# Kernel optimization log

Measured on AMD Instinct MI355X. Metric: run time of the kernel, lower is better.

The kernel has to match this reference:

```python
import jax, jax.numpy as jnp
import numpy as np

D_MODEL = 1024
N_HEADS = 16


def setup_inputs() -> dict:
    key = jax.random.key(0)
    ks = jax.random.split(key, 5)
    sigma = (1.0 / D_MODEL) ** 0.5
    return {
        "x": jax.random.normal(ks[0], (4, 2048, D_MODEL), dtype=jnp.float32),
        "W_q": jax.random.normal(ks[1], (D_MODEL, D_MODEL), dtype=jnp.float32) * sigma,
        "W_k": jax.random.normal(ks[2], (D_MODEL, D_MODEL), dtype=jnp.float32) * sigma,
        "W_v": jax.random.normal(ks[3], (D_MODEL, D_MODEL), dtype=jnp.float32) * sigma,
        "W_o": jax.random.normal(ks[4], (D_MODEL, D_MODEL), dtype=jnp.float32) * sigma,
    }


def reference(x, W_q, W_k, W_v, W_o):
    b, s, d = x.shape
    h = N_HEADS
    d_h = d // h
    # Projections: original does einsum('d_out dim, ... dim -> ... d_out') == x @ W.T
    def proj(W):
        y = jnp.einsum('bsd,ed->bse', x, W)
        # ... seq (head d_h) -> ... head seq d_h
        return y.reshape(b, s, h, d_h).transpose(0, 2, 1, 3)
    Q, K, V = proj(W_q), proj(W_k), proj(W_v)
    scale = 1.0 / jnp.sqrt(jnp.asarray(d_h, dtype=x.dtype))
    scores = jnp.einsum('bhqd,bhkd->bhqk', Q, K) * scale  # [b,h,s,s]
    causal = jnp.tril(jnp.ones((s, s), dtype=bool))
    scores = jnp.where(causal, scores, -jnp.inf)
    attn = jax.nn.softmax(scores, axis=-1)
    out = jnp.einsum('bhqk,bhkd->bhqd', attn, V)  # [b,h,s,d_h]
    out = out.transpose(0, 2, 1, 3).reshape(b, s, d)
    # einsum(Temp, W_o, '... dim1, dim dim1 -> ... dim') == Temp @ W_o.T
    return jnp.einsum('bse,de->bsd', out, W_o)
```

## Files before the change

### kernel.cpp

```cpp
#include <hip/hip_runtime.h>

typedef __attribute__((ext_vector_type(8))) short s16x8;
typedef __attribute__((ext_vector_type(4))) short s16x4;
typedef __attribute__((ext_vector_type(4))) float f32x4;
typedef unsigned short u16;
typedef unsigned int u32;
typedef unsigned long long u64;

__device__ __forceinline__ u16 f2bf(float f) {
  unsigned u = __builtin_bit_cast(unsigned, f);
  return (u16)((u + 0x7fffu + ((u >> 16) & 1u)) >> 16);
}

#define QSCALE 0.18033688011112042f

__device__ __forceinline__ void gld16(const u16* g, u16* l) {
  __builtin_amdgcn_global_load_lds(
      (const __attribute__((address_space(1))) void*)g,
      (__attribute__((address_space(3))) void*)l, 16, 0, 0);
}

__device__ __forceinline__ u32 pack_trunc(float a, float b) {
  return __builtin_amdgcn_perm(__builtin_bit_cast(u32, b),
                               __builtin_bit_cast(u32, a), 0x07060302u);
}

__global__ __launch_bounds__(256)
void cvt_bf16(const float* __restrict__ src, u16* __restrict__ dst, int n8)
{
  const int i = blockIdx.x * 256 + threadIdx.x;
  if (i < n8) {
    f32x4 a = ((const f32x4*)src)[2 * i];
    f32x4 b = ((const f32x4*)src)[2 * i + 1];
    s16x8 pk;
    pk[0] = (short)f2bf(a[0]); pk[1] = (short)f2bf(a[1]);
    pk[2] = (short)f2bf(a[2]); pk[3] = (short)f2bf(a[3]);
    pk[4] = (short)f2bf(b[0]); pk[5] = (short)f2bf(b[1]);
    pk[6] = (short)f2bf(b[2]); pk[7] = (short)f2bf(b[3]);
    ((s16x8*)dst)[i] = pk;
  }
}

template<bool OUT_QKV>
__global__ __launch_bounds__(256)
void gemm97(const u16* __restrict__ A,
            const u16* __restrict__ B0, const u16* __restrict__ B1,
            const u16* __restrict__ B2,
            u16* __restrict__ o0, u16* __restrict__ o1, u16* __restrict__ o2,
            float* __restrict__ oF)
{
  const int by = blockIdx.x;
  const int bx = blockIdx.y;
  const int bz = blockIdx.z;
  const u16* B = (bz == 0) ? B0 : ((bz == 1) ? B1 : B2);
  u16* oQ = (bz == 0) ? o0 : ((bz == 1) ? o1 : o2);

  __shared__ u16 As[128 * 32];
  __shared__ u16 Bs[128 * 32];

  const int tid  = threadIdx.x;
  const int w    = tid >> 6;
  const int lane = tid & 63;
  const int quad = lane >> 4;
  const int l15  = lane & 15;
  const int wm   = (w >> 1) * 64;
  const int wn   = (w & 1) * 64;

  const int arb  = w * 32;
  const int srow = lane >> 2;
  const int scol = (lane & 3) * 8;
  const u16* ga = A + (size_t)(by * 128 + arb + srow) * 1024 + scol;
  const u16* gb = B + (size_t)(bx * 128 + arb + srow) * 1024 + scol;
  u16* la0 = &As[arb * 32];
  u16* la1 = &As[(arb + 16) * 32];
  u16* lb0 = &Bs[arb * 32];
  u16* lb1 = &Bs[(arb + 16) * 32];

  f32x4 acc[4][4];
  #pragma unroll
  for (int i = 0; i < 4; ++i)
    #pragma unroll
    for (int j = 0; j < 4; ++j)
      acc[i][j] = (f32x4){0.f, 0.f, 0.f, 0.f};

  for (int k0 = 0; k0 < 1024; k0 += 32) {
    gld16(ga + k0,               la0);
    gld16(ga + k0 + 16 * 1024,   la1);
    gld16(gb + k0,               lb0);
    gld16(gb + k0 + 16 * 1024,   lb1);
    __syncthreads();

    s16x8 af[4], bf[4];
    #pragma unroll
    for (int i = 0; i < 4; ++i)
      af[i] = *(const s16x8*)&As[(wm + i * 16 + l15) * 32 + quad * 8];
    #pragma unroll
    for (int i = 0; i < 4; ++i)
      bf[i] = *(const s16x8*)&Bs[(wn + i * 16 + l15) * 32 + quad * 8];
    #pragma unroll
    for (int mt = 0; mt < 4; ++mt)
      #pragma unroll
      for (int nt = 0; nt < 4; ++nt)
        acc[mt][nt] = __builtin_amdgcn_mfma_f32_16x16x32_bf16(
            af[mt], bf[nt], acc[mt][nt], 0, 0, 0);
    __syncthreads();
  }

  #pragma unroll
  for (int mt = 0; mt < 4; ++mt)
    #pragma unroll
    for (int nt = 0; nt < 4; ++nt)
      #pragma unroll
      for (int r = 0; r < 4; ++r) {
        const int row = by * 128 + wm + mt * 16 + quad * 4 + r;
        const int col = bx * 128 + wn + nt * 16 + l15;
        float v = acc[mt][nt][r];
        if (OUT_QKV) {
          if (bz == 0) v *= QSCALE;
          const int b = row >> 11, s = row & 2047, hh = col >> 6, d = col & 63;
          oQ[(size_t)(b * 16 + hh) * 131072 + s * 64 + d] = f2bf(v);
        } else {
          oF[(size_t)row * 1024 + col] = v;
        }
      }
}

__global__ __launch_bounds__(256)
void vtrans(const u16* __restrict__ Vb, u16* __restrict__ VT)
{
  const int st = blockIdx.x;
  const int bh = blockIdx.y;
  __shared__ u16 T[64 * 72];
  const int tid = threadIdx.x;
  const size_t base = (size_t)bh * 131072;
  #pragma unroll
  for (int p = 0; p < 2; ++p) {
    const int idx = tid + p * 256;
    const int row = idx >> 3;
    const int col = (idx & 7) * 8;
    s16x8 v = *(const s16x8*)(Vb + base + (size_t)(st * 64 + row) * 64 + col);
    #pragma unroll
    for (int e = 0; e < 8; ++e) T[(col + e) * 72 + row] = v[e];
  }
  __syncthreads();
  #pragma unroll
  for (int p = 0; p < 2; ++p) {
    const int idx = tid + p * 256;
    const int drow = idx >> 3;
    const int scol = (idx & 7) * 8;
    *(s16x8*)(VT + base + (size_t)drow * 2048 + st * 64 + scol) =
        *(const s16x8*)&T[drow * 72 + scol];
  }
}

#define ATTN_STEP(t, Pw, qtt)                                                  \
  do {                                                                         \
    f32x4 S[4];                                                                \
    _Pragma("unroll")                                                          \
    for (int nt = 0; nt < 4; ++nt) {                                           \
      s16x8 b0 = *(const s16x8*)&Ks[(nt * 16 + l15) * 72 + quad * 8];          \
      s16x8 b1 = *(const s16x8*)&Ks[(nt * 16 + l15) * 72 + 32 + quad * 8];     \
      f32x4 z = (f32x4){0.f, 0.f, 0.f, 0.f};                                   \
      z = __builtin_amdgcn_mfma_f32_16x16x32_bf16(aq[t][0], b0, z, 0, 0, 0);   \
      z = __builtin_amdgcn_mfma_f32_16x16x32_bf16(aq[t][1], b1, z, 0, 0, 0);   \
      S[nt] = z;                                                               \
    }                                                                          \
    if (j == (qtt)) {                                                          \
      _Pragma("unroll")                                                        \
      for (int nt = 0; nt < 4; ++nt)                                           \
        _Pragma("unroll")                                                      \
        for (int r = 0; r < 4; ++r) {                                          \
          const int kg = 4 * l15 + nt;                                         \
          const int qg = w * 16 + quad * 4 + r;                                \
          if (kg > qg) S[nt][r] = -1e30f;                                      \
        }                                                                      \
    }                                                                          \
    _Pragma("unroll")                                                          \
    for (int r = 0; r < 4; ++r) {                                              \
      float rm = fmaxf(fmaxf(S[0][r], S[1][r]), fmaxf(S[2][r], S[3][r]));      \
      _Pragma("unroll")                                                        \
      for (int off = 1; off < 16; off <<= 1)                                   \
        rm = fmaxf(rm, __shfl_xor(rm, off, 64));                               \
      const float mold = mi[t][r];                                             \
      const float mnew = fmaxf(mold, rm);                                      \
      const float alpha = __builtin_amdgcn_exp2f(mold - mnew);                 \
      mi[t][r] = mnew;                                                         \
      const float p0 = __builtin_amdgcn_exp2f(S[0][r] - mnew);                 \
      const float p1 = __builtin_amdgcn_exp2f(S[1][r] - mnew);                 \
      const float p2 = __builtin_amdgcn_exp2f(S[2][r] - mnew);                 \
      const float p3 = __builtin_amdgcn_exp2f(S[3][r] - mnew);                 \
      liacc[t][r] *= alpha;                                                    \
      _Pragma("unroll")                                                        \
      for (int dt = 0; dt < 4; ++dt) O[t][dt][r] *= alpha;                     \
      const u64 pk = (u64)pack_trunc(p0, p1) |                                 \
                     ((u64)pack_trunc(p2, p3) << 32);                          \
      *(u64*)&(Pw)[(quad * 4 + r) * 72 + 4 * l15] = pk;                        \
    }                                                                          \
    s16x8 a0 = *(const s16x8*)&(Pw)[l15 * 72 + quad * 8];                      \
    s16x8 a1 = *(const s16x8*)&(Pw)[l15 * 72 + 32 + quad * 8];                 \
    liacc[t] = __builtin_amdgcn_mfma_f32_16x16x32_bf16(a0, ones, liacc[t], 0, 0, 0); \
    liacc[t] = __builtin_amdgcn_mfma_f32_16x16x32_bf16(a1, ones, liacc[t], 0, 0, 0); \
    _Pragma("unroll")                                                          \
    for (int dt = 0; dt < 4; ++dt) {                                           \
      s16x8 b0 = *(const s16x8*)&Vt[(dt * 16 + l15) * 72 + quad * 8];          \
      s16x8 b1 = *(const s16x8*)&Vt[(dt * 16 + l15) * 72 + 32 + quad * 8];     \
      O[t][dt] = __builtin_amdgcn_mfma_f32_16x16x32_bf16(a0, b0, O[t][dt], 0, 0, 0); \
      O[t][dt] = __builtin_amdgcn_mfma_f32_16x16x32_bf16(a1, b1, O[t][dt], 0, 0, 0); \
    }                                                                          \
  } while (0)

__global__ __launch_bounds__(256, 4)
void attn_kernel(const u16* __restrict__ Qg, const u16* __restrict__ Kg,
                 const u16* __restrict__ VTg, u16* __restrict__ out)
{
  const int pi = blockIdx.x;
  const int bh = blockIdx.y;
  const int b = bh >> 4, h = bh & 15;
  const int qt0 = 31 - pi;
  const int qt1 = pi;

  __shared__ u16 Qs[128 * 72];
  __shared__ u16 Ks[64 * 72];
  __shared__ u16 Vt[64 * 72];

  const int tid = threadIdx.x;
  const int w = tid >> 6, lane = tid & 63, quad = lane >> 4, l15 = lane & 15;
  const size_t base = (size_t)bh * 131072;

  {
    const int col = (tid & 7) * 8;
    #pragma unroll
    for (int p = 0; p < 4; ++p) {
      const int row = (tid >> 3) + p * 32;
      const int gq = (row < 64) ? (qt0 * 64 + row) : (qt1 * 64 + (row - 64));
      *(s16x8*)&Qs[row * 72 + col] =
          *(const s16x8*)(Qg + base + (size_t)gq * 64 + col);
    }
  }
  __syncthreads();

  s16x8 aq[2][2];
  #pragma unroll
  for (int t = 0; t < 2; ++t)
    #pragma unroll
    for (int ks = 0; ks < 2; ++ks)
      aq[t][ks] = *(const s16x8*)&Qs[(t * 64 + w * 16 + l15) * 72 + ks * 32 + quad * 8];

  u16* Pw0 = &Qs[(w * 16) * 72];
  u16* Pw1 = &Qs[(64 + w * 16) * 72];

  s16x8 ones;
  #pragma unroll
  for (int e = 0; e < 8; ++e) ones[e] = (short)0x3F80;

  f32x4 O[2][4], liacc[2];
  float mi[2][4];
  #pragma unroll
  for (int t = 0; t < 2; ++t) {
    #pragma unroll
    for (int dt = 0; dt < 4; ++dt) O[t][dt] = (f32x4){0.f, 0.f, 0.f, 0.f};
    liacc[t] = (f32x4){0.f, 0.f, 0.f, 0.f};
    #pragma unroll
    for (int r = 0; r < 4; ++r) mi[t][r] = -1e30f;
  }

  for (int j = 0; j <= qt0; ++j) {
    #pragma unroll
    for (int p = 0; p < 2; ++p) {
      const int idx = tid + p * 256;
      const int key = idx >> 3, col = (idx & 7) * 8;
      const int slot = (key & 3) * 16 + (key >> 2);
      *(s16x8*)&Ks[slot * 72 + col] =
          *(const s16x8*)(Kg + base + (size_t)(j * 64 + key) * 64 + col);
    }
    #pragma unroll
    for (int p = 0; p < 2; ++p) {
      const int idx = tid + p * 256;
      const int d = idx >> 3, col = (idx & 7) * 8;
      *(s16x8*)&Vt[d * 72 + col] =
          *(const s16x8*)(VTg + base + (size_t)d * 2048 + j * 64 + col);
    }
    __syncthreads();

    ATTN_STEP(0, Pw0, qt0);
    if (j <= qt1) ATTN_STEP(1, Pw1, qt1);
    __syncthreads();
  }

  #pragma unroll
  for (int t = 0; t < 2; ++t) {
    const int qtt = t ? qt1 : qt0;
    #pragma unroll
    for (int r = 0; r < 4; ++r) {
      const float inv = __builtin_amdgcn_rcpf(liacc[t][r]);
      const int sq = qtt * 64 + w * 16 + quad * 4 + r;
      #pragma unroll
      for (int dt = 0; dt < 4; ++dt)
        out[(size_t)(b * 2048 + sq) * 1024 + h * 64 + dt * 16 + l15] =
            f2bf(O[t][dt][r] * inv);
    }
  }
}

extern "C" void kernel_launch(void* const* d_in, const int* in_sizes, int n_in,
                              void* d_out, int out_size, void* d_ws, size_t ws_size,
                              hipStream_t stream) {
  (void)in_sizes; (void)n_in; (void)out_size; (void)ws_size;
  const float* x  = (const float*)d_in[0];
  const float* Wq = (const float*)d_in[1];
  const float* Wk = (const float*)d_in[2];
  const float* Wv = (const float*)d_in[3];
  const float* Wo = (const float*)d_in[4];
  float* out = (float*)d_out;

  u16* W16 = (u16*)d_ws;
  u16* xb  = W16;
  u16* VT  = W16;
  u16* Qb  = W16 + 8388608;
  u16* Kb  = W16 + 16777216;
  u16* Vb  = W16 + 25165824;
  u16* AO  = Vb;
  u16* Wqb = W16 + 33554432;
  u16* Wkb = Wqb + 1048576;
  u16* Wvb = Wkb + 1048576;
  u16* Wob = Wvb + 1048576;

  dim3 blk(256);
  cvt_bf16<<<dim3(4096), blk, 0, stream>>>(x,  xb,  1048576);
  cvt_bf16<<<dim3(512),  blk, 0, stream>>>(Wq, Wqb, 131072);
  cvt_bf16<<<dim3(512),  blk, 0, stream>>>(Wk, Wkb, 131072);
  cvt_bf16<<<dim3(512),  blk, 0, stream>>>(Wv, Wvb, 131072);
  cvt_bf16<<<dim3(512),  blk, 0, stream>>>(Wo, Wob, 131072);

  gemm97<true ><<<dim3(64, 8, 3), blk, 0, stream>>>(
      xb, Wqb, Wkb, Wvb, Qb, Kb, Vb, nullptr);
  vtrans<<<dim3(32, 64), blk, 0, stream>>>(Vb, VT);
  attn_kernel<<<dim3(16, 64), blk, 0, stream>>>(Qb, Kb, VT, AO);
  gemm97<false><<<dim3(64, 8, 1), blk, 0, stream>>>(
      AO, Wob, Wob, Wob, nullptr, nullptr, nullptr, out);
}
```

Baseline: 284.2 us.

## Write V transposed from GEMM, fuse conversions, use direct-to-LDS loads in attention

Merges the five fp32-to-bf16 conversion launches into one kernel and drops the separate V transpose kernel by having the QKV GEMM epilogue write V directly in transposed layout. The attention kernel now loads K and V^T tiles with global_load_lds into a split unpadded layout, and shrinks the Q/P padding stride. This removes launch overhead and a full pass over V, but the transposed epilogue store is strided and poorly coalesced, and the new strides may cause LDS bank conflicts.

After: 301.8 us. 1.06x slower.

```diff
diff --git a/kernel.cpp b/kernel.cpp
--- a/kernel.cpp
+++ b/kernel.cpp
@@ -26,19 +26,27 @@
 }
 
 __global__ __launch_bounds__(256)
-void cvt_bf16(const float* __restrict__ src, u16* __restrict__ dst, int n8)
+void cvt_all(const float* __restrict__ x,  u16* __restrict__ xb,
+             const float* __restrict__ w0, u16* __restrict__ w0b,
+             const float* __restrict__ w1, u16* __restrict__ w1b,
+             const float* __restrict__ w2, u16* __restrict__ w2b,
+             const float* __restrict__ w3, u16* __restrict__ w3b)
 {
-  const int i = blockIdx.x * 256 + threadIdx.x;
-  if (i < n8) {
-    f32x4 a = ((const f32x4*)src)[2 * i];
-    f32x4 b = ((const f32x4*)src)[2 * i + 1];
-    s16x8 pk;
-    pk[0] = (short)f2bf(a[0]); pk[1] = (short)f2bf(a[1]);
-    pk[2] = (short)f2bf(a[2]); pk[3] = (short)f2bf(a[3]);
-    pk[4] = (short)f2bf(b[0]); pk[5] = (short)f2bf(b[1]);
-    pk[6] = (short)f2bf(b[2]); pk[7] = (short)f2bf(b[3]);
-    ((s16x8*)dst)[i] = pk;
-  }
+  int bb = blockIdx.x;
+  const float* src; u16* dst; int i;
+  if (bb < 4096)      { src = x;  dst = xb;  i = bb * 256 + threadIdx.x; }
+  else if (bb < 4608) { src = w0; dst = w0b; i = (bb - 4096) * 256 + threadIdx.x; }
+  else if (bb < 5120) { src = w1; dst = w1b; i = (bb - 4608) * 256 + threadIdx.x; }
+  else if (bb < 5632) { src = w2; dst = w2b; i = (bb - 5120) * 256 + threadIdx.x; }
+  else                { src = w3; dst = w3b; i = (bb - 5632) * 256 + threadIdx.x; }
+  f32x4 a = ((const f32x4*)src)[2 * i];
+  f32x4 b = ((const f32x4*)src)[2 * i + 1];
+  s16x8 pk;
+  pk[0] = (short)f2bf(a[0]); pk[1] = (short)f2bf(a[1]);
+  pk[2] = (short)f2bf(a[2]); pk[3] = (short)f2bf(a[3]);
+  pk[4] = (short)f2bf(b[0]); pk[5] = (short)f2bf(b[1]);
+  pk[6] = (short)f2bf(b[2]); pk[7] = (short)f2bf(b[3]);
+  ((s16x8*)dst)[i] = pk;
 }
 
 template<bool OUT_QKV>
@@ -116,41 +124,17 @@
         const int col = bx * 128 + wn + nt * 16 + l15;
         float v = acc[mt][nt][r];
         if (OUT_QKV) {
-          if (bz == 0) v *= QSCALE;
           const int b = row >> 11, s = row & 2047, hh = col >> 6, d = col & 63;
-          oQ[(size_t)(b * 16 + hh) * 131072 + s * 64 + d] = f2bf(v);
+          if (bz == 2) {
+            oQ[(size_t)(b * 16 + hh) * 131072 + d * 2048 + s] = f2bf(v);
+          } else {
+            if (bz == 0) v *= QSCALE;
+            oQ[(size_t)(b * 16 + hh) * 131072 + s * 64 + d] = f2bf(v);
+          }
         } else {
           oF[(size_t)row * 1024 + col] = v;
         }
       }
-}
-
-__global__ __launch_bounds__(256)
-void vtrans(const u16* __restrict__ Vb, u16* __restrict__ VT)
-{
-  const int st = blockIdx.x;
-  const int bh = blockIdx.y;
-  __shared__ u16 T[64 * 72];
-  const int tid = threadIdx.x;
-  const size_t base = (size_t)bh * 131072;
-  #pragma unroll
-  for (int p = 0; p < 2; ++p) {
-    const int idx = tid + p * 256;
-    const int row = idx >> 3;
-    const int col = (idx & 7) * 8;
-    s16x8 v = *(const s16x8*)(Vb + base + (size_t)(st * 64 + row) * 64 + col);
-    #pragma unroll
-    for (int e = 0; e < 8; ++e) T[(col + e) * 72 + row] = v[e];
-  }
-  __syncthreads();
-  #pragma unroll
-  for (int p = 0; p < 2; ++p) {
-    const int idx = tid + p * 256;
-    const int drow = idx >> 3;
-    const int scol = (idx & 7) * 8;
-    *(s16x8*)(VT + base + (size_t)drow * 2048 + st * 64 + scol) =
-        *(const s16x8*)&T[drow * 72 + scol];
-  }
 }
 
 #define ATTN_STEP(t, Pw, qtt)                                                  \
@@ -158,8 +142,8 @@
     f32x4 S[4];                                                                \
     _Pragma("unroll")                                                          \
     for (int nt = 0; nt < 4; ++nt) {                                           \
-      s16x8 b0 = *(const s16x8*)&Ks[(nt * 16 + l15) * 72 + quad * 8];          \
-      s16x8 b1 = *(const s16x8*)&Ks[(nt * 16 + l15) * 72 + 32 + quad * 8];     \
+      s16x8 b0 = *(const s16x8*)&Ks[(nt * 16 + l15) * 32 + quad * 8];          \
+      s16x8 b1 = *(const s16x8*)&Ks[2048 + (nt * 16 + l15) * 32 + quad * 8];   \
       f32x4 z = (f32x4){0.f, 0.f, 0.f, 0.f};                                   \
       z = __builtin_amdgcn_mfma_f32_16x16x32_bf16(aq[t][0], b0, z, 0, 0, 0);   \
       z = __builtin_amdgcn_mfma_f32_16x16x32_bf16(aq[t][1], b1, z, 0, 0, 0);   \
@@ -194,16 +178,16 @@
       for (int dt = 0; dt < 4; ++dt) O[t][dt][r] *= alpha;                     \
       const u64 pk = (u64)pack_trunc(p0, p1) |                                 \
                      ((u64)pack_trunc(p2, p3) << 32);                          \
-      *(u64*)&(Pw)[(quad * 4 + r) * 72 + 4 * l15] = pk;                        \
+      *(u64*)&(Pw)[(quad * 4 + r) * 68 + 4 * l15] = pk;                        \
     }                                                                          \
-    s16x8 a0 = *(const s16x8*)&(Pw)[l15 * 72 + quad * 8];                      \
-    s16x8 a1 = *(const s16x8*)&(Pw)[l15 * 72 + 32 + quad * 8];                 \
+    s16x8 a0 = *(const s16x8*)&(Pw)[l15 * 68 + quad * 8];                      \
+    s16x8 a1 = *(const s16x8*)&(Pw)[l15 * 68 + 32 + quad * 8];                 \
     liacc[t] = __builtin_amdgcn_mfma_f32_16x16x32_bf16(a0, ones, liacc[t], 0, 0, 0); \
     liacc[t] = __builtin_amdgcn_mfma_f32_16x16x32_bf16(a1, ones, liacc[t], 0, 0, 0); \
     _Pragma("unroll")                                                          \
     for (int dt = 0; dt < 4; ++dt) {                                           \
-      s16x8 b0 = *(const s16x8*)&Vt[(dt * 16 + l15) * 72 + quad * 8];          \
-      s16x8 b1 = *(const s16x8*)&Vt[(dt * 16 + l15) * 72 + 32 + quad * 8];     \
+      s16x8 b0 = *(const s16x8*)&Vt[(dt * 16 + l15) * 32 + quad * 8];          \
+      s16x8 b1 = *(const s16x8*)&Vt[2048 + (dt * 16 + l15) * 32 + quad * 8];   \
       O[t][dt] = __builtin_amdgcn_mfma_f32_16x16x32_bf16(a0, b0, O[t][dt], 0, 0, 0); \
       O[t][dt] = __builtin_amdgcn_mfma_f32_16x16x32_bf16(a1, b1, O[t][dt], 0, 0, 0); \
     }                                                                          \
@@ -219,9 +203,9 @@
   const int qt0 = 31 - pi;
   const int qt1 = pi;
 
-  __shared__ u16 Qs[128 * 72];
-  __shared__ u16 Ks[64 * 72];
-  __shared__ u16 Vt[64 * 72];
+  __shared__ u16 Qs[128 * 68];
+  __shared__ u16 Ks[2 * 64 * 32];
+  __shared__ u16 Vt[2 * 64 * 32];
 
   const int tid = threadIdx.x;
   const int w = tid >> 6, lane = tid & 63, quad = lane >> 4, l15 = lane & 15;
@@ -233,7 +217,7 @@
     for (int p = 0; p < 4; ++p) {
       const int row = (tid >> 3) + p * 32;
       const int gq = (row < 64) ? (qt0 * 64 + row) : (qt1 * 64 + (row - 64));
-      *(s16x8*)&Qs[row * 72 + col] =
+      *(s16x8*)&Qs[row * 68 + col] =
           *(const s16x8*)(Qg + base + (size_t)gq * 64 + col);
     }
   }
@@ -244,10 +228,10 @@
   for (int t = 0; t < 2; ++t)
     #pragma unroll
     for (int ks = 0; ks < 2; ++ks)
-      aq[t][ks] = *(const s16x8*)&Qs[(t * 64 + w * 16 + l15) * 72 + ks * 32 + quad * 8];
-
-  u16* Pw0 = &Qs[(w * 16) * 72];
-  u16* Pw1 = &Qs[(64 + w * 16) * 72];
+      aq[t][ks] = *(const s16x8*)&Qs[(t * 64 + w * 16 + l15) * 68 + ks * 32 + quad * 8];
+
+  u16* Pw0 = &Qs[(w * 16) * 68];
+  u16* Pw1 = &Qs[(64 + w * 16) * 68];
 
   s16x8 ones;
   #pragma unroll
@@ -264,22 +248,23 @@
     for (int r = 0; r < 4; ++r) mi[t][r] = -1e30f;
   }
 
+  const int kkey   = (lane >> 2) * 4 + w;
+  const int vd     = w * 16 + (lane >> 2);
+  const int chunk  = (lane & 3) * 8;
+  const u16* gk = Kg  + base + (size_t)kkey * 64 + chunk;
+  const u16* gv = VTg + base + (size_t)vd * 2048 + chunk;
+  u16* lk0 = &Ks[w * 16 * 32];
+  u16* lk1 = &Ks[2048 + w * 16 * 32];
+  u16* lv0 = &Vt[w * 16 * 32];
+  u16* lv1 = &Vt[2048 + w * 16 * 32];
+
   for (int j = 0; j <= qt0; ++j) {
-    #pragma unroll
-    for (int p = 0; p < 2; ++p) {
-      const int idx = tid + p * 256;
-      const int key = idx >> 3, col = (idx & 7) * 8;
-      const int slot = (key & 3) * 16 + (key >> 2);
-      *(s16x8*)&Ks[slot * 72 + col] =
-          *(const s16x8*)(Kg + base + (size_t)(j * 64 + key) * 64 + col);
-    }
-    #pragma unroll
-    for (int p = 0; p < 2; ++p) {
-      const int idx = tid + p * 256;
-      const int d = idx >> 3, col = (idx & 7) * 8;
-      *(s16x8*)&Vt[d * 72 + col] =
-          *(const s16x8*)(VTg + base + (size_t)d * 2048 + j * 64 + col);
-    }
+    const size_t koff = (size_t)j * 4096;
+    const size_t voff = (size_t)j * 64;
+    gld16(gk + koff,      lk0);
+    gld16(gk + koff + 32, lk1);
+    gld16(gv + voff,      lv0);
+    gld16(gv + voff + 32, lv1);
     __syncthreads();
 
     ATTN_STEP(0, Pw0, qt0);
@@ -315,26 +300,20 @@
 
   u16* W16 = (u16*)d_ws;
   u16* xb  = W16;
-  u16* VT  = W16;
+  u16* AO  = W16;
   u16* Qb  = W16 + 8388608;
   u16* Kb  = W16 + 16777216;
-  u16* Vb  = W16 + 25165824;
-  u16* AO  = Vb;
+  u16* VT  = W16 + 25165824;
   u16* Wqb = W16 + 33554432;
   u16* Wkb = Wqb + 1048576;
   u16* Wvb = Wkb + 1048576;
   u16* Wob = Wvb + 1048576;
 
   dim3 blk(256);
-  cvt_bf16<<<dim3(4096), blk, 0, stream>>>(x,  xb,  1048576);
-  cvt_bf16<<<dim3(512),  blk, 0, stream>>>(Wq, Wqb, 131072);
-  cvt_bf16<<<dim3(512),  blk, 0, stream>>>(Wk, Wkb, 131072);
-  cvt_bf16<<<dim3(512),  blk, 0, stream>>>(Wv, Wvb, 131072);
-  cvt_bf16<<<dim3(512),  blk, 0, stream>>>(Wo, Wob, 131072);
-
+  cvt_all<<<dim3(6144), blk, 0, stream>>>(x, xb, Wq, Wqb, Wk, Wkb,
+                                          Wv, Wvb, Wo, Wob);
   gemm97<true ><<<dim3(64, 8, 3), blk, 0, stream>>>(
-      xb, Wqb, Wkb, Wvb, Qb, Kb, Vb, nullptr);
-  vtrans<<<dim3(32, 64), blk, 0, stream>>>(Vb, VT);
+      xb, Wqb, Wkb, Wvb, Qb, Kb, VT, nullptr);
   attn_kernel<<<dim3(16, 64), blk, 0, stream>>>(Qb, Kb, VT, AO);
   gemm97<false><<<dim3(64, 8, 1), blk, 0, stream>>>(
       AO, Wob, Wob, Wob, nullptr, nullptr, nullptr, out);
```
